# Kernel optimization log

Hardware: AMD Instinct MI355X
Metric: run time of the kernel (lower is better)

The kernel has to match this reference:

```python
import jax, jax.numpy as jnp
import numpy as np

NHEAD = 8


def _global_query_attention(cs, ks, vs):
    """cs: (B,H,G,Ek) global queries; ks: (B,H,S,Ek); vs: (B,H,S,Ev).
    For each key position i: v'_i = sum_{s<=i} softmax(K[:i] @ q) * V[:i].
    Returns (B,H,S,G,Ev)."""
    w = jnp.exp(jnp.einsum('bhge,bhse->bhgs', cs, ks))          # (B,H,G,S)
    norms = jnp.cumsum(w, axis=-1)                               # (B,H,G,S)
    wv = w[..., None] * vs[:, :, None, :, :]                     # (B,H,G,S,Ev) -- huge intermediate
    resp = jnp.cumsum(wv, axis=-2) / norms[..., None]            # (B,H,G,S,Ev)
    return jnp.swapaxes(resp, -3, -2)                            # (B,H,S,G,Ev)


def setup_inputs() -> dict:
    B, L, E, G = 4, 2048, 512, 16
    KD = VD = E
    keys = jax.random.split(jax.random.key(0), 9)
    s_qk = 0.02              # keep exp(q.k) finite in fp32
    s_v = 1.0 / np.sqrt(VD).astype(np.float32)
    return {
        'query':        jax.random.normal(keys[0], (B, L, E), jnp.float32),
        'key':          jax.random.normal(keys[1], (B, L, E), jnp.float32),
        'value':        jax.random.normal(keys[2], (B, L, E), jnp.float32),
        'context':      jax.random.normal(keys[3], (B, G, E), jnp.float32),
        'query_proj':   jax.random.normal(keys[4], (1, E, KD), jnp.float32) * s_qk,
        'key_proj':     jax.random.normal(keys[5], (1, E, KD), jnp.float32) * s_qk,
        'value_proj':   jax.random.normal(keys[6], (1, E, VD), jnp.float32) * s_v,
        'output_proj':  jax.random.normal(keys[7], (1, VD, E), jnp.float32) * s_v,
        'context_proj': jax.random.normal(keys[8], (1, E, KD), jnp.float32) * s_qk,
    }


def reference(query, key, value, context, query_proj, key_proj, value_proj, output_proj, context_proj):
    B, L, E = query.shape
    G = context.shape[1]
    H = NHEAD
    KD = query_proj.shape[-1]
    VD = value_proj.shape[-1]
    Ek, Ev = KD // H, VD // H

    def heads(x, W, n, dh):
        # (B,n,E) @ (1,E,D) -> (B,n,D) -> (B,H,n,dh)
        return jnp.swapaxes((x @ W).reshape(B, n, H, dh), 1, 2)

    cs = heads(context, context_proj, G, Ek)   # (B,H,G,Ek)
    qs = heads(query, query_proj, L, Ek)       # (B,H,L,Ek)
    ks = heads(key, key_proj, L, Ek)           # (B,H,S,Ek)
    vs = heads(value, value_proj, L, Ev)       # (B,H,S,Ev)

    resp_v = _global_query_attention(cs, ks, vs)   # (B,H,S,G,Ev)
    resp_k = _global_query_attention(cs, ks, ks)   # (B,H,S,G,Ek)

    logits = jnp.einsum('bhse,bhsge->bhsg', qs, resp_k)   # (B,H,S,G)
    w = jax.nn.softmax(logits, axis=-1)
    out = jnp.einsum('bhsg,bhsge->bhse', w, resp_v)       # (B,H,S,Ev)
    out = jnp.swapaxes(out, 1, 2).reshape(B, L, VD)       # (B,S,vdim)
    return out @ output_proj                               # (B,S,d_model)
```

## Files before the change

### kernel.cpp

```cpp
#include <hip/hip_runtime.h>
#include <hip/hip_bf16.h>

#define NB 4
#define SL 2048
#define NG 16
#define NH 8
#define DH 64
#define NBH (NB * NH)
#define NCH (SL / 64)

typedef __attribute__((ext_vector_type(8))) short bh8;
typedef __attribute__((ext_vector_type(4))) float fx4;

__device__ __forceinline__ ushort f2bf(float x) {
    union { float f; unsigned u; } v; v.f = x;
    const unsigned r = v.u + 0x7fffu + ((v.u >> 16) & 1u);
    return (ushort)(r >> 16);
}
__device__ __forceinline__ float b2f(ushort u) {
    union { unsigned u; float f; } v; v.u = ((unsigned)u) << 16;
    return v.f;
}
__device__ __forceinline__ bh8 pack8(float4 lo, float4 hi) {
    bh8 r;
    r[0] = (short)f2bf(lo.x); r[1] = (short)f2bf(lo.y);
    r[2] = (short)f2bf(lo.z); r[3] = (short)f2bf(lo.w);
    r[4] = (short)f2bf(hi.x); r[5] = (short)f2bf(hi.y);
    r[6] = (short)f2bf(hi.z); r[7] = (short)f2bf(hi.w);
    return r;
}
__device__ __forceinline__ void unpack8(bh8 v, float4& lo, float4& hi) {
    lo.x = b2f((ushort)v[0]); lo.y = b2f((ushort)v[1]);
    lo.z = b2f((ushort)v[2]); lo.w = b2f((ushort)v[3]);
    hi.x = b2f((ushort)v[4]); hi.y = b2f((ushort)v[5]);
    hi.z = b2f((ushort)v[6]); hi.w = b2f((ushort)v[7]);
}
__device__ __forceinline__ int swz(int row, int col) {
    return row * 64 + (col ^ ((row & 7) << 3));
}

__global__ __launch_bounds__(256) void convT512_4(const float* __restrict__ w0,
                                                  const float* __restrict__ w1,
                                                  const float* __restrict__ w2,
                                                  const float* __restrict__ w3,
                                                  ushort* __restrict__ o0,
                                                  ushort* __restrict__ o1,
                                                  ushort* __restrict__ o2,
                                                  ushort* __restrict__ o3) {
    const int z = blockIdx.z;
    const float* W = (z == 0) ? w0 : (z == 1) ? w1 : (z == 2) ? w2 : w3;
    ushort* WT = (z == 0) ? o0 : (z == 1) ? o1 : (z == 2) ? o2 : o3;
    __shared__ float tile[32][33];
    const int bx = blockIdx.x * 32, by = blockIdx.y * 32;
    const int tx = threadIdx.x & 31, ty = threadIdx.x >> 5;
#pragma unroll
    for (int p = 0; p < 4; ++p)
        tile[ty + p * 8][tx] = W[(size_t)(by + ty + p * 8) * 512 + bx + tx];
    __syncthreads();
#pragma unroll
    for (int p = 0; p < 4; ++p)
        WT[(size_t)(bx + ty + p * 8) * 512 + by + tx] = f2bf(tile[tx][ty + p * 8]);
}

__global__ __launch_bounds__(256, 3) void gemm_qkv_kernel(
    const float* __restrict__ qf, const float* __restrict__ kf,
    const float* __restrict__ vf, const ushort* __restrict__ qpT,
    const ushort* __restrict__ kpT, const ushort* __restrict__ vpT,
    ushort* __restrict__ qsb, ushort* __restrict__ ksb, ushort* __restrict__ vsb) {
    const int z = blockIdx.z;
    const float* A32 = (z == 0) ? qf : (z == 1) ? kf : vf;
    const ushort* BT = (z == 0) ? qpT : (z == 1) ? kpT : vpT;
    ushort* out = (z == 0) ? qsb : (z == 1) ? ksb : vsb;

    __shared__ __align__(16) ushort As[2][64 * 64];
    __shared__ __align__(16) ushort Bs[2][128 * 64];
    const int t = threadIdx.x;
    const int lane = t & 63, w = t >> 6;
    const int bm = blockIdx.x * 64, bn = blockIdx.y * 128;
    const int ar = t >> 2, ao = (t & 3) * 16;
    const size_t abase = (size_t)(bm + ar) * 512 + ao;
    const int asw0 = swz(ar, ao), asw1 = swz(ar, ao + 8);
    size_t bsrc[4];
#pragma unroll
    for (int i = 0; i < 4; ++i) {
        const int s = w * 2048 + i * 512 + lane * 8;
        const int r = s >> 6, o = (s & 63) ^ ((r & 7) << 3);
        bsrc[i] = (size_t)(bn + r) * 512 + o;
    }
    const int wr = w >> 1, wc = w & 1;
    const int fr = lane & 15, kg = lane >> 4;
    fx4 acc[2][4] = {};
    float4 a0v, a1v, a2v, a3v;

#define LOADA(kk)                                                              \
    do {                                                                       \
        a0v = *(const float4*)&A32[abase + (kk)];                              \
        a1v = *(const float4*)&A32[abase + (kk) + 4];                          \
        a2v = *(const float4*)&A32[abase + (kk) + 8];                          \
        a3v = *(const float4*)&A32[abase + (kk) + 12];                         \
    } while (0)
#define WRITEA(buf)                                                            \
    do {                                                                       \
        *(bh8*)&As[buf][asw0] = pack8(a0v, a1v);                               \
        *(bh8*)&As[buf][asw1] = pack8(a2v, a3v);                               \
    } while (0)
#define STAGEB(buf, kk)                                                        \
    do {                                                                       \
        _Pragma("unroll")                                                      \
        for (int i = 0; i < 4; ++i)                                            \
            __builtin_amdgcn_global_load_lds(                                  \
                (const __attribute__((address_space(1))) void*)(BT + bsrc[i] + (kk)), \
                (__attribute__((address_space(3))) void*)&Bs[buf][w * 2048 + i * 512], \
                16, 0, 0);                                                     \
    } while (0)

    LOADA(0);
    STAGEB(0, 0);
    WRITEA(0);
    LOADA(64);
    __syncthreads();
    int cur = 0;
    for (int k0 = 0; k0 < 512; k0 += 64) {
        if (k0 + 64 < 512) {
            STAGEB(cur ^ 1, k0 + 64);
            WRITEA(cur ^ 1);
            if (k0 + 128 < 512) LOADA(k0 + 128);
        }
#pragma unroll
        for (int kk = 0; kk < 2; ++kk) {
            bh8 af[2], bf[4];
#pragma unroll
            for (int m = 0; m < 2; ++m) {
                const int R = wr * 32 + m * 16 + fr;
                af[m] = *(const bh8*)&As[cur][swz(R, kk * 32 + kg * 8)];
            }
#pragma unroll
            for (int nn = 0; nn < 4; ++nn) {
                const int C = wc * 64 + nn * 16 + fr;
                bf[nn] = *(const bh8*)&Bs[cur][swz(C, kk * 32 + kg * 8)];
            }
#pragma unroll
            for (int m = 0; m < 2; ++m)
#pragma unroll
                for (int nn = 0; nn < 4; ++nn)
                    acc[m][nn] = __builtin_amdgcn_mfma_f32_16x16x32_bf16(
                        af[m], bf[nn], acc[m][nn], 0, 0, 0);
        }
        __syncthreads();
        cur ^= 1;
    }
#undef LOADA
#undef WRITEA
#undef STAGEB
#pragma unroll
    for (int m = 0; m < 2; ++m)
#pragma unroll
        for (int nn = 0; nn < 4; ++nn)
#pragma unroll
            for (int j = 0; j < 4; ++j) {
                const int r = bm + wr * 32 + m * 16 + kg * 4 + j;
                const int cc = bn + wc * 64 + nn * 16 + fr;
                const int b = r >> 11, i = r & 2047;
                out[(((size_t)(b * NH) + (cc >> 6)) * SL + i) * DH + (cc & 63)] =
                    f2bf(acc[m][nn][j]);
            }
}

__global__ __launch_bounds__(256, 3) void gemm_out_kernel(const ushort* __restrict__ A,
                                                          const ushort* __restrict__ BT,
                                                          float* __restrict__ out) {
    __shared__ __align__(16) ushort As[2][64 * 64];
    __shared__ __align__(16) ushort Bs[2][128 * 64];
    const int t = threadIdx.x;
    const int lane = t & 63, w = t >> 6;
    const int bm = blockIdx.x * 64, bn = blockIdx.y * 128;
    size_t asrc[2], bsrc[4];
#pragma unroll
    for (int i = 0; i < 2; ++i) {
        const int s = w * 1024 + i * 512 + lane * 8;
        const int r = s >> 6, o = (s & 63) ^ ((r & 7) << 3);
        asrc[i] = (size_t)(bm + r) * 512 + o;
    }
#pragma unroll
    for (int i = 0; i < 4; ++i) {
        const int s = w * 2048 + i * 512 + lane * 8;
        const int r = s >> 6, o = (s & 63) ^ ((r & 7) << 3);
        bsrc[i] = (size_t)(bn + r) * 512 + o;
    }
    const int wr = w >> 1, wc = w & 1;
    const int fr = lane & 15, kg = lane >> 4;
    fx4 acc[2][4] = {};

#define STAGE_O(buf, kk)                                                       \
    do {                                                                       \
        _Pragma("unroll")                                                      \
        for (int i = 0; i < 2; ++i)                                            \
            __builtin_amdgcn_global_load_lds(                                  \
                (const __attribute__((address_space(1))) void*)(A + asrc[i] + (kk)), \
                (__attribute__((address_space(3))) void*)&As[buf][w * 1024 + i * 512], \
                16, 0, 0);                                                     \
        _Pragma("unroll")                                                      \
        for (int i = 0; i < 4; ++i)                                            \
            __builtin_amdgcn_global_load_lds(                                  \
                (const __attribute__((address_space(1))) void*)(BT + bsrc[i] + (kk)), \
                (__attribute__((address_space(3))) void*)&Bs[buf][w * 2048 + i * 512], \
                16, 0, 0);                                                     \
    } while (0)

    STAGE_O(0, 0);
    __syncthreads();
    int cur = 0;
    for (int k0 = 0; k0 < 512; k0 += 64) {
        if (k0 + 64 < 512) STAGE_O(cur ^ 1, k0 + 64);
#pragma unroll
        for (int kk = 0; kk < 2; ++kk) {
            bh8 af[2], bf[4];
#pragma unroll
            for (int m = 0; m < 2; ++m) {
                const int R = wr * 32 + m * 16 + fr;
                af[m] = *(const bh8*)&As[cur][swz(R, kk * 32 + kg * 8)];
            }
#pragma unroll
            for (int nn = 0; nn < 4; ++nn) {
                const int C = wc * 64 + nn * 16 + fr;
                bf[nn] = *(const bh8*)&Bs[cur][swz(C, kk * 32 + kg * 8)];
            }
#pragma unroll
            for (int m = 0; m < 2; ++m)
#pragma unroll
                for (int nn = 0; nn < 4; ++nn)
                    acc[m][nn] = __builtin_amdgcn_mfma_f32_16x16x32_bf16(
                        af[m], bf[nn], acc[m][nn], 0, 0, 0);
        }
        __syncthreads();
        cur ^= 1;
    }
#undef STAGE_O
#pragma unroll
    for (int m = 0; m < 2; ++m)
#pragma unroll
        for (int nn = 0; nn < 4; ++nn)
#pragma unroll
            for (int j = 0; j < 4; ++j) {
                const int r = bm + wr * 32 + m * 16 + kg * 4 + j;
                const int cc = bn + wc * 64 + nn * 16 + fr;
                out[(size_t)r * 512 + cc] = acc[m][nn][j];
            }
}

template <int MODE>
__global__ __launch_bounds__(256) void gemm512(const float* __restrict__ X,
                                               const float* __restrict__ Wm,
                                               float* __restrict__ out, int n) {
    __shared__ float As[16][65];
    __shared__ float Bs[16][64];
    const int t = threadIdx.x;
    const int rm = blockIdx.x * 64;
    const int cn = blockIdx.y * 64;
    const int tm = t >> 4, tn = t & 15;
    const int arow = t >> 2, ak = (t & 3) << 2;
    const int bk = t >> 4, bc = (t & 15) << 2;
    float acc[4][4] = {};
    for (int k0 = 0; k0 < 512; k0 += 16) {
        float4 av = *(const float4*)&X[(size_t)(rm + arow) * 512 + k0 + ak];
        float4 bv = *(const float4*)&Wm[(size_t)(k0 + bk) * 512 + cn + bc];
        __syncthreads();
        As[ak + 0][arow] = av.x;
        As[ak + 1][arow] = av.y;
        As[ak + 2][arow] = av.z;
        As[ak + 3][arow] = av.w;
        *(float4*)&Bs[bk][bc] = bv;
        __syncthreads();
#pragma unroll
        for (int kk = 0; kk < 16; ++kk) {
            float a0 = As[kk][tm * 4 + 0], a1 = As[kk][tm * 4 + 1];
            float a2 = As[kk][tm * 4 + 2], a3 = As[kk][tm * 4 + 3];
            float4 b = *(const float4*)&Bs[kk][tn * 4];
            acc[0][0] += a0 * b.x; acc[0][1] += a0 * b.y; acc[0][2] += a0 * b.z; acc[0][3] += a0 * b.w;
            acc[1][0] += a1 * b.x; acc[1][1] += a1 * b.y; acc[1][2] += a1 * b.z; acc[1][3] += a1 * b.w;
            acc[2][0] += a2 * b.x; acc[2][1] += a2 * b.y; acc[2][2] += a2 * b.z; acc[2][3] += a2 * b.w;
            acc[3][0] += a3 * b.x; acc[3][1] += a3 * b.y; acc[3][2] += a3 * b.z; acc[3][3] += a3 * b.w;
        }
    }
#pragma unroll
    for (int j = 0; j < 4; ++j) {
        const int r = rm + tm * 4 + j;
#pragma unroll
        for (int jj = 0; jj < 4; ++jj) {
            const int cc = cn + tn * 4 + jj;
            if (MODE == 0) {
                const int b = r / n, i = r % n;
                out[(((size_t)(b * NH) + (cc >> 6)) * n + i) * DH + (cc & 63)] = acc[j][jj];
            } else {
                out[(size_t)r * 512 + cc] = acc[j][jj];
            }
        }
    }
}

__global__ __launch_bounds__(256) void chunk_sums_w_kernel(
    const ushort* __restrict__ ksb, const ushort* __restrict__ vsb,
    const float* __restrict__ cs, float* __restrict__ wb,
    float* __restrict__ wbT, float* __restrict__ Mc, float* __restrict__ Nc) {
    const int bh = blockIdx.x, c = blockIdx.y;
    __shared__ float Ks[64 * 64];
    __shared__ float Vs[64 * 64];
    __shared__ float Ws[64 * 16];
    __shared__ float Cs[16][65];
    const int t = threadIdx.x;
    const ushort* kbase = ksb + ((size_t)bh * SL + c * 64) * DH;
    const ushort* vbase = vsb + ((size_t)bh * SL + c * 64) * DH;
#pragma unroll
    for (int p = 0; p < 2; ++p) {
        const int idx = (p * 256 + t) * 8;
        float4 lo, hi;
        unpack8(*(const bh8*)&kbase[idx], lo, hi);
        *(float4*)&Ks[idx] = lo; *(float4*)&Ks[idx + 4] = hi;
        unpack8(*(const bh8*)&vbase[idx], lo, hi);
        *(float4*)&Vs[idx] = lo; *(float4*)&Vs[idx + 4] = hi;
    }
    {
        const int idx = t * 4;
        const float4 cv = *(const float4*)&cs[(size_t)bh * NG * DH + idx];
        const int g = idx >> 6, e = idx & 63;
        Cs[g][e + 0] = cv.x; Cs[g][e + 1] = cv.y; Cs[g][e + 2] = cv.z; Cs[g][e + 3] = cv.w;
    }
    __syncthreads();
    {
        const int i = (t * 4) >> 4, g0 = (t * 4) & 15;
        float d0 = 0.f, d1 = 0.f, d2 = 0.f, d3 = 0.f;
#pragma unroll 8
        for (int e = 0; e < 64; ++e) {
            const float kv = Ks[i * 64 + e];
            d0 += kv * Cs[g0 + 0][e];
            d1 += kv * Cs[g0 + 1][e];
            d2 += kv * Cs[g0 + 2][e];
            d3 += kv * Cs[g0 + 3][e];
        }
        float4 wv;
        wv.x = expf(d0); wv.y = expf(d1); wv.z = expf(d2); wv.w = expf(d3);
        *(float4*)&Ws[i * 16 + g0] = wv;
        *(float4*)&wb[((size_t)bh * SL + c * 64 + i) * NG + g0] = wv;
    }
    __syncthreads();
    {
        const int g = t >> 4, i0 = (t & 15) * 4;
        float4 wv4;
        wv4.x = Ws[(i0 + 0) * 16 + g];
        wv4.y = Ws[(i0 + 1) * 16 + g];
        wv4.z = Ws[(i0 + 2) * 16 + g];
        wv4.w = Ws[(i0 + 3) * 16 + g];
        *(float4*)&wbT[((size_t)(bh * NG) + g) * SL + c * 64 + i0] = wv4;
    }
    const int e = t >> 2, g0 = (t & 3) * 4;
    float m0 = 0.f, m1 = 0.f, m2 = 0.f, m3 = 0.f;
#pragma unroll 8
    for (int i = 0; i < 64; ++i) {
        const float kv = Ks[i * 64 + e];
        const float4 w = *(const float4*)&Ws[i * 16 + g0];
        m0 += kv * w.x; m1 += kv * w.y; m2 += kv * w.z; m3 += kv * w.w;
    }
    const int g2 = t >> 4, e2 = (t & 15) * 4;
    float n0 = 0.f, n1 = 0.f, n2 = 0.f, n3 = 0.f;
#pragma unroll 8
    for (int i = 0; i < 64; ++i) {
        const float wv = Ws[i * 16 + g2];
        const float4 vv = *(const float4*)&Vs[i * 64 + e2];
        n0 += wv * vv.x; n1 += wv * vv.y; n2 += wv * vv.z; n3 += wv * vv.w;
    }
    float* mo = Mc + ((size_t)(bh * NCH + c) * 64 + e) * 16 + g0;
    mo[0] = m0; mo[1] = m1; mo[2] = m2; mo[3] = m3;
    float* no = Nc + ((size_t)(bh * NCH + c) * 16 + g2) * 64 + e2;
    no[0] = n0; no[1] = n1; no[2] = n2; no[3] = n3;
}

__global__ __launch_bounds__(256) void scans_kernel(const float* __restrict__ wbT,
                                                    float* __restrict__ nb,
                                                    float* __restrict__ Mc,
                                                    float* __restrict__ Nc) {
    const int bid = blockIdx.x;
    const int t = threadIdx.x;
    if (bid < NBH * NG) {
        __shared__ float sw[2048];
        __shared__ float sp[256];
#pragma unroll
        for (int p = 0; p < 2; ++p) {
            const int idx = (p * 256 + t) * 4;
            *(float4*)&sw[idx] = *(const float4*)&wbT[(size_t)bid * SL + idx];
        }
        __syncthreads();
        float loc[8];
        float run = 0.f;
#pragma unroll
        for (int j = 0; j < 8; ++j) { run += sw[t * 8 + j]; loc[j] = run; }
        sp[t] = run;
        __syncthreads();
        for (int off = 1; off < 256; off <<= 1) {
            const float v = sp[t];
            const float add = (t >= off) ? sp[t - off] : 0.f;
            __syncthreads();
            sp[t] = v + add;
            __syncthreads();
        }
        const float offs = (t > 0) ? sp[t - 1] : 0.f;
#pragma unroll
        for (int j = 0; j < 8; ++j)
            nb[(size_t)bid * SL + t * 8 + j] = offs + loc[j];
    } else {
        const int idx = bid - NBH * NG;
        const int bh = idx >> 1;
        float* base = ((idx & 1) ? Nc : Mc) + (size_t)bh * NCH * 1024;
        float4 run = make_float4(0.f, 0.f, 0.f, 0.f);
        float4 nxt = *(float4*)&base[t * 4];
        for (int c = 0; c < NCH; ++c) {
            const float4 v = nxt;
            if (c + 1 < NCH) nxt = *(float4*)&base[(c + 1) * 1024 + t * 4];
            *(float4*)&base[c * 1024 + t * 4] = run;
            run.x += v.x; run.y += v.y; run.z += v.z; run.w += v.w;
        }
    }
}

__global__ __launch_bounds__(256) void pass1c_kernel(const ushort* __restrict__ qsb,
                                                     const ushort* __restrict__ ksb,
                                                     const float* __restrict__ wb,
                                                     const float* __restrict__ nb,
                                                     const float* __restrict__ Mc,
                                                     float* __restrict__ cb) {
    const int bh = blockIdx.x;
    const int r = blockIdx.y;
    const int s0 = r * 64;
    __shared__ float Qs[64][65];
    __shared__ float Kt[64][65];
    __shared__ float At[64][65];
    __shared__ float Wt[64 * 16];
    __shared__ float Pt[64 * 16];
    __shared__ float Lg[64][17];
    const int t = threadIdx.x;
    const int am = t >> 4, an = t & 15;
    const ushort* qbase = qsb + ((size_t)bh * SL + s0) * DH;
    const ushort* kbase = ksb + ((size_t)bh * SL + s0) * DH;
#pragma unroll
    for (int p = 0; p < 2; ++p) {
        const int idx = (p * 256 + t) * 8;
        const int row = idx >> 6, col = idx & 63;
        float4 lo, hi;
        unpack8(*(const bh8*)&qbase[idx], lo, hi);
        *(float4*)&Qs[row][col] = lo; *(float4*)&Qs[row][col + 4] = hi;
        unpack8(*(const bh8*)&kbase[idx], lo, hi);
        *(float4*)&Kt[row][col] = lo; *(float4*)&Kt[row][col + 4] = hi;
    }
    *(float4*)&Wt[t * 4] = *(const float4*)&wb[((size_t)bh * SL + s0) * NG + t * 4];
    *(float4*)&Pt[t * 4] = *(const float4*)&Mc[(size_t)(bh * NCH + r) * 1024 + t * 4];
    __syncthreads();
    float a[4][4] = {};
#pragma unroll 8
    for (int e = 0; e < 64; ++e) {
        float qv[4], kv[4];
#pragma unroll
        for (int j = 0; j < 4; ++j) qv[j] = Qs[am * 4 + j][e];
#pragma unroll
        for (int jj = 0; jj < 4; ++jj) kv[jj] = Kt[an * 4 + jj][e];
#pragma unroll
        for (int j = 0; j < 4; ++j)
#pragma unroll
            for (int jj = 0; jj < 4; ++jj) a[j][jj] += qv[j] * kv[jj];
    }
#pragma unroll
    for (int j = 0; j < 4; ++j)
#pragma unroll
        for (int jj = 0; jj < 4; ++jj) {
            if (an * 4 + jj > am * 4 + j) a[j][jj] = 0.f;
            At[am * 4 + j][an * 4 + jj] = a[j][jj];
        }
    __syncthreads();
    float lg[4] = {0.f, 0.f, 0.f, 0.f};
#pragma unroll 8
    for (int ii = 0; ii < 64; ++ii) {
        const float wv = Wt[ii * 16 + an];
#pragma unroll
        for (int j = 0; j < 4; ++j) lg[j] += At[am * 4 + j][ii] * wv;
    }
#pragma unroll 8
    for (int e = 0; e < 64; ++e) {
        const float pv = Pt[e * 16 + an];
#pragma unroll
        for (int j = 0; j < 4; ++j) lg[j] += Qs[am * 4 + j][e] * pv;
    }
#pragma unroll
    for (int j = 0; j < 4; ++j) Lg[am * 4 + j][an] = lg[j];
    __syncthreads();
    if (t < 64) {
        const int s = s0 + t;
        const float* nbase = nb + (size_t)bh * NG * SL + s;
        float nv[16], l[16];
        float mx = -1e30f;
#pragma unroll
        for (int g = 0; g < 16; ++g) {
            nv[g] = nbase[(size_t)g * SL];
            l[g] = Lg[t][g] / nv[g];
            mx = fmaxf(mx, l[g]);
        }
        float sum = 0.f;
#pragma unroll
        for (int g = 0; g < 16; ++g) { l[g] = expf(l[g] - mx); sum += l[g]; }
        const float inv = 1.f / sum;
#pragma unroll
        for (int g = 0; g < 16; ++g)
            cb[((size_t)bh * SL + s) * NG + g] = l[g] * inv / nv[g];
    }
}

__global__ __launch_bounds__(256) void pass2c_kernel(const float* __restrict__ cb,
                                                     const float* __restrict__ wb,
                                                     const ushort* __restrict__ vsb,
                                                     const float* __restrict__ Nc,
                                                     ushort* __restrict__ ohb) {
    const int bh = blockIdx.x;
    const int b = bh >> 3, h = bh & 7;
    const int r = blockIdx.y;
    const int s0 = r * 64;
    __shared__ float Ct[64][17];
    __shared__ float Wt[64][17];
    __shared__ float Vt[64 * 64];
    __shared__ float St[64][65];
    __shared__ float Ut[16 * 64];
    const int t = threadIdx.x;
    const int am = t >> 4, an = t & 15;
    {
        const int idx = t * 4;
        const int row = idx >> 4, g0 = idx & 15;
        const float4 cv = *(const float4*)&cb[((size_t)bh * SL + s0) * NG + idx];
        Ct[row][g0 + 0] = cv.x; Ct[row][g0 + 1] = cv.y;
        Ct[row][g0 + 2] = cv.z; Ct[row][g0 + 3] = cv.w;
        const float4 wv = *(const float4*)&wb[((size_t)bh * SL + s0) * NG + idx];
        Wt[row][g0 + 0] = wv.x; Wt[row][g0 + 1] = wv.y;
        Wt[row][g0 + 2] = wv.z; Wt[row][g0 + 3] = wv.w;
    }
    const ushort* vbase = vsb + ((size_t)bh * SL + s0) * DH;
#pragma unroll
    for (int p = 0; p < 2; ++p) {
        const int idx = (p * 256 + t) * 8;
        float4 lo, hi;
        unpack8(*(const bh8*)&vbase[idx], lo, hi);
        *(float4*)&Vt[idx] = lo; *(float4*)&Vt[idx + 4] = hi;
    }
    *(float4*)&Ut[t * 4] = *(const float4*)&Nc[(size_t)(bh * NCH + r) * 1024 + t * 4];
    __syncthreads();
    float sv[4][4] = {};
#pragma unroll
    for (int g = 0; g < 16; ++g) {
        float cv[4], wv[4];
#pragma unroll
        for (int j = 0; j < 4; ++j) cv[j] = Ct[am * 4 + j][g];
#pragma unroll
        for (int jj = 0; jj < 4; ++jj) wv[jj] = Wt[an * 4 + jj][g];
#pragma unroll
        for (int j = 0; j < 4; ++j)
#pragma unroll
            for (int jj = 0; jj < 4; ++jj) sv[j][jj] += cv[j] * wv[jj];
    }
#pragma unroll
    for (int j = 0; j < 4; ++j)
#pragma unroll
        for (int jj = 0; jj < 4; ++jj) {
            if (an * 4 + jj > am * 4 + j) sv[j][jj] = 0.f;
            St[am * 4 + j][an * 4 + jj] = sv[j][jj];
        }
    __syncthreads();
    float acc[4][4] = {};
#pragma unroll
    for (int g = 0; g < 16; ++g) {
        const float4 u = *(const float4*)&Ut[g * 64 + an * 4];
        float cv[4];
#pragma unroll
        for (int j = 0; j < 4; ++j) cv[j] = Ct[am * 4 + j][g];
#pragma unroll
        for (int j = 0; j < 4; ++j) {
            acc[j][0] += cv[j] * u.x; acc[j][1] += cv[j] * u.y;
            acc[j][2] += cv[j] * u.z; acc[j][3] += cv[j] * u.w;
        }
    }
#pragma unroll 8
    for (int ii = 0; ii < 64; ++ii) {
        const float4 vv = *(const float4*)&Vt[ii * 64 + an * 4];
        float st[4];
#pragma unroll
        for (int j = 0; j < 4; ++j) st[j] = St[am * 4 + j][ii];
#pragma unroll
        for (int j = 0; j < 4; ++j) {
            acc[j][0] += st[j] * vv.x; acc[j][1] += st[j] * vv.y;
            acc[j][2] += st[j] * vv.z; acc[j][3] += st[j] * vv.w;
        }
    }
#pragma unroll
    for (int j = 0; j < 4; ++j) {
        const int s = s0 + am * 4 + j;
        ushort4 pk;
        pk.x = f2bf(acc[j][0]); pk.y = f2bf(acc[j][1]);
        pk.z = f2bf(acc[j][2]); pk.w = f2bf(acc[j][3]);
        *(ushort4*)&ohb[((size_t)b * SL + s) * 512 + h * DH + an * 4] = pk;
    }
}

extern "C" void kernel_launch(void* const* d_in, const int* in_sizes, int n_in,
                              void* d_out, int out_size, void* d_ws, size_t ws_size,
                              hipStream_t stream) {
    const float* query   = (const float*)d_in[0];
    const float* key     = (const float*)d_in[1];
    const float* value   = (const float*)d_in[2];
    const float* context = (const float*)d_in[3];
    const float* qp = (const float*)d_in[4];
    const float* kp = (const float*)d_in[5];
    const float* vp = (const float*)d_in[6];
    const float* op = (const float*)d_in[7];
    const float* cp = (const float*)d_in[8];
    float* out = (float*)d_out;

    ushort* qsb = (ushort*)d_ws;
    ushort* ksb = qsb + 4194304;
    ushort* vsb = ksb + 4194304;
    ushort* ohb = vsb + 4194304;
    ushort* qpT = ohb + 4194304;
    ushort* kpT = qpT + 262144;
    ushort* vpT = kpT + 262144;
    ushort* opT = vpT + 262144;
    float* fbase = (float*)(opT + 262144);
    float* cs = fbase;
    float* wb = cs + 32768;
    float* nb = wb + 1048576;
    float* Mc = nb + 1048576;
    float* Nc = Mc + 1048576;
    float* cb = Nc + 1048576;
    float* wbT = cb + 1048576;

    dim3 blk(256);
    convT512_4<<<dim3(16, 16, 4), blk, 0, stream>>>(qp, kp, vp, op, qpT, kpT, vpT, opT);
    gemm512<0><<<dim3(1, 8), blk, 0, stream>>>(context, cp, cs, NG);
    gemm_qkv_kernel<<<dim3(128, 4, 3), blk, 0, stream>>>(query, key, value,
                                                         qpT, kpT, vpT, qsb, ksb, vsb);
    chunk_sums_w_kernel<<<dim3(NBH, NCH), blk, 0, stream>>>(ksb, vsb, cs, wb, wbT, Mc, Nc);
    scans_kernel<<<dim3(NBH * NG + NBH * 2), blk, 0, stream>>>(wbT, nb, Mc, Nc);
    pass1c_kernel<<<dim3(NBH, NCH), blk, 0, stream>>>(qsb, ksb, wb, nb, Mc, cb);
    pass2c_kernel<<<dim3(NBH, NCH), blk, 0, stream>>>(cb, wb, vsb, Nc, ohb);
    gemm_out_kernel<<<dim3(128, 4), blk, 0, stream>>>(ohb, opT, out);
}
```

Baseline: 150.3 us.

## Deepen GEMM prefetch with manual waitcnt barriers and fuse context projection into prep

Merges the context-projection GEMM into the weight transpose/convert kernel as an extra grid slice, which removes one kernel launch. In the QKV and output GEMMs it replaces __syncthreads double buffering with a two-stage prefetch. Each iteration issues the next tile's global loads after the barrier and uses explicit s_waitcnt vmcnt counts and raw s_barrier, so global latency overlaps MFMA work. The hand-tuned vmcnt counts depend on exact instruction counts, and a wrong count could race or stall.

Result: faster. 145.4 us (-3.3%).

```diff
diff --git a/kernel.cpp b/kernel.cpp
--- a/kernel.cpp
+++ b/kernel.cpp
@@ -39,27 +39,69 @@
     return row * 64 + (col ^ ((row & 7) << 3));
 }
 
-__global__ __launch_bounds__(256) void convT512_4(const float* __restrict__ w0,
-                                                  const float* __restrict__ w1,
-                                                  const float* __restrict__ w2,
-                                                  const float* __restrict__ w3,
-                                                  ushort* __restrict__ o0,
-                                                  ushort* __restrict__ o1,
-                                                  ushort* __restrict__ o2,
-                                                  ushort* __restrict__ o3) {
+__global__ __launch_bounds__(256) void prep_kernel(
+    const float* __restrict__ w0, const float* __restrict__ w1,
+    const float* __restrict__ w2, const float* __restrict__ w3,
+    const float* __restrict__ cp, const float* __restrict__ context,
+    ushort* __restrict__ o0, ushort* __restrict__ o1,
+    ushort* __restrict__ o2, ushort* __restrict__ o3,
+    float* __restrict__ cs) {
     const int z = blockIdx.z;
-    const float* W = (z == 0) ? w0 : (z == 1) ? w1 : (z == 2) ? w2 : w3;
-    ushort* WT = (z == 0) ? o0 : (z == 1) ? o1 : (z == 2) ? o2 : o3;
-    __shared__ float tile[32][33];
-    const int bx = blockIdx.x * 32, by = blockIdx.y * 32;
-    const int tx = threadIdx.x & 31, ty = threadIdx.x >> 5;
-#pragma unroll
-    for (int p = 0; p < 4; ++p)
-        tile[ty + p * 8][tx] = W[(size_t)(by + ty + p * 8) * 512 + bx + tx];
-    __syncthreads();
-#pragma unroll
-    for (int p = 0; p < 4; ++p)
-        WT[(size_t)(bx + ty + p * 8) * 512 + by + tx] = f2bf(tile[tx][ty + p * 8]);
+    const int t = threadIdx.x;
+    if (z < 4) {
+        const float* W = (z == 0) ? w0 : (z == 1) ? w1 : (z == 2) ? w2 : w3;
+        ushort* WT = (z == 0) ? o0 : (z == 1) ? o1 : (z == 2) ? o2 : o3;
+        __shared__ float tile[32][33];
+        const int bx = blockIdx.x * 32, by = blockIdx.y * 32;
+        const int tx = t & 31, ty = t >> 5;
+#pragma unroll
+        for (int p = 0; p < 4; ++p)
+            tile[ty + p * 8][tx] = W[(size_t)(by + ty + p * 8) * 512 + bx + tx];
+        __syncthreads();
+#pragma unroll
+        for (int p = 0; p < 4; ++p)
+            WT[(size_t)(bx + ty + p * 8) * 512 + by + tx] = f2bf(tile[tx][ty + p * 8]);
+    } else {
+        if (blockIdx.x != 0 || blockIdx.y >= 8) return;
+        __shared__ float As[16][65];
+        __shared__ float Bs[16][64];
+        const int cn = blockIdx.y * 64;
+        const int tm = t >> 4, tn = t & 15;
+        const int arow = t >> 2, ak = (t & 3) << 2;
+        const int bk = t >> 4, bc = (t & 15) << 2;
+        float acc[4][4] = {};
+        for (int k0 = 0; k0 < 512; k0 += 16) {
+            float4 av = *(const float4*)&context[(size_t)arow * 512 + k0 + ak];
+            float4 bv = *(const float4*)&cp[(size_t)(k0 + bk) * 512 + cn + bc];
+            __syncthreads();
+            As[ak + 0][arow] = av.x;
+            As[ak + 1][arow] = av.y;
+            As[ak + 2][arow] = av.z;
+            As[ak + 3][arow] = av.w;
+            *(float4*)&Bs[bk][bc] = bv;
+            __syncthreads();
+#pragma unroll
+            for (int kk = 0; kk < 16; ++kk) {
+                float a0 = As[kk][tm * 4 + 0], a1 = As[kk][tm * 4 + 1];
+                float a2 = As[kk][tm * 4 + 2], a3 = As[kk][tm * 4 + 3];
+                float4 b = *(const float4*)&Bs[kk][tn * 4];
+                acc[0][0] += a0 * b.x; acc[0][1] += a0 * b.y; acc[0][2] += a0 * b.z; acc[0][3] += a0 * b.w;
+                acc[1][0] += a1 * b.x; acc[1][1] += a1 * b.y; acc[1][2] += a1 * b.z; acc[1][3] += a1 * b.w;
+                acc[2][0] += a2 * b.x; acc[2][1] += a2 * b.y; acc[2][2] += a2 * b.z; acc[2][3] += a2 * b.w;
+                acc[3][0] += a3 * b.x; acc[3][1] += a3 * b.y; acc[3][2] += a3 * b.z; acc[3][3] += a3 * b.w;
+            }
+        }
+#pragma unroll
+        for (int j = 0; j < 4; ++j) {
+            const int r = tm * 4 + j;
+#pragma unroll
+            for (int jj = 0; jj < 4; ++jj) {
+                const int cc = cn + tn * 4 + jj;
+                const int b = r / NG, i = r % NG;
+                cs[(((size_t)(b * NH) + (cc >> 6)) * NG + i) * DH + (cc & 63)] = acc[j][jj];
+            }
+        }
+    }
 }
 
 __global__ __launch_bounds__(256, 3) void gemm_qkv_kernel(
@@ -113,45 +155,60 @@
                 (__attribute__((address_space(3))) void*)&Bs[buf][w * 2048 + i * 512], \
                 16, 0, 0);                                                     \
     } while (0)
+#define MFMA_PHASE(buf)                                                        \
+    do {                                                                       \
+        _Pragma("unroll")                                                      \
+        for (int kk = 0; kk < 2; ++kk) {                                       \
+            bh8 af[2], bf[4];                                                  \
+            _Pragma("unroll")                                                  \
+            for (int m = 0; m < 2; ++m) {                                      \
+                const int R = wr * 32 + m * 16 + fr;                           \
+                af[m] = *(const bh8*)&As[buf][swz(R, kk * 32 + kg * 8)];       \
+            }                                                                  \
+            _Pragma("unroll")                                                  \
+            for (int nn = 0; nn < 4; ++nn) {                                   \
+                const int C = wc * 64 + nn * 16 + fr;                          \
+                bf[nn] = *(const bh8*)&Bs[buf][swz(C, kk * 32 + kg * 8)];      \
+            }                                                                  \
+            _Pragma("unroll")                                                  \
+            for (int m = 0; m < 2; ++m)                                        \
+                _Pragma("unroll")                                              \
+                for (int nn = 0; nn < 4; ++nn)                                 \
+                    acc[m][nn] = __builtin_amdgcn_mfma_f32_16x16x32_bf16(      \
+                        af[m], bf[nn], acc[m][nn], 0, 0, 0);                   \
+        }                                                                      \
+    } while (0)
 
     LOADA(0);
     STAGEB(0, 0);
     WRITEA(0);
+    STAGEB(1, 64);
     LOADA(64);
-    __syncthreads();
+    asm volatile("s_waitcnt vmcnt(8) lgkmcnt(0)" ::: "memory");
+    __builtin_amdgcn_s_barrier();
+    __builtin_amdgcn_sched_barrier(0);
+
     int cur = 0;
     for (int k0 = 0; k0 < 512; k0 += 64) {
-        if (k0 + 64 < 512) {
-            STAGEB(cur ^ 1, k0 + 64);
-            WRITEA(cur ^ 1);
-            if (k0 + 128 < 512) LOADA(k0 + 128);
-        }
-#pragma unroll
-        for (int kk = 0; kk < 2; ++kk) {
-            bh8 af[2], bf[4];
-#pragma unroll
-            for (int m = 0; m < 2; ++m) {
-                const int R = wr * 32 + m * 16 + fr;
-                af[m] = *(const bh8*)&As[cur][swz(R, kk * 32 + kg * 8)];
-            }
-#pragma unroll
-            for (int nn = 0; nn < 4; ++nn) {
-                const int C = wc * 64 + nn * 16 + fr;
-                bf[nn] = *(const bh8*)&Bs[cur][swz(C, kk * 32 + kg * 8)];
-            }
-#pragma unroll
-            for (int m = 0; m < 2; ++m)
-#pragma unroll
-                for (int nn = 0; nn < 4; ++nn)
-                    acc[m][nn] = __builtin_amdgcn_mfma_f32_16x16x32_bf16(
-                        af[m], bf[nn], acc[m][nn], 0, 0, 0);
-        }
-        __syncthreads();
+        MFMA_PHASE(cur);
+        if (k0 + 64 < 512) WRITEA(cur ^ 1);
+        asm volatile("s_waitcnt lgkmcnt(0)" ::: "memory");
+        __builtin_amdgcn_s_barrier();
+        __builtin_amdgcn_sched_barrier(0);
+        if (k0 + 128 < 512) {
+            STAGEB(cur, k0 + 128);
+            LOADA(k0 + 128);
+            asm volatile("s_waitcnt vmcnt(8)" ::: "memory");
+        } else if (k0 + 64 < 512) {
+            asm volatile("s_waitcnt vmcnt(0)" ::: "memory");
+        }
+        __builtin_amdgcn_sched_barrier(0);
         cur ^= 1;
     }
 #undef LOADA
 #undef WRITEA
 #undef STAGEB
+#undef MFMA_PHASE
 #pragma unroll
     for (int m = 0; m < 2; ++m)
 #pragma unroll
@@ -208,10 +265,12 @@
     } while (0)
 
     STAGE_O(0, 0);
-    __syncthreads();
+    STAGE_O(1, 64);
+    asm volatile("s_waitcnt vmcnt(6)" ::: "memory");
+    __builtin_amdgcn_s_barrier();
+    __builtin_amdgcn_sched_barrier(0);
     int cur = 0;
     for (int k0 = 0; k0 < 512; k0 += 64) {
-        if (k0 + 64 < 512) STAGE_O(cur ^ 1, k0 + 64);
 #pragma unroll
         for (int kk = 0; kk < 2; ++kk) {
             bh8 af[2], bf[4];
@@ -232,7 +291,16 @@
                     acc[m][nn] = __builtin_amdgcn_mfma_f32_16x16x32_bf16(
                         af[m], bf[nn], acc[m][nn], 0, 0, 0);
         }
-        __syncthreads();
+        asm volatile("s_waitcnt lgkmcnt(0)" ::: "memory");
+        __builtin_amdgcn_s_barrier();
+        __builtin_amdgcn_sched_barrier(0);
+        if (k0 + 128 < 512) {
+            STAGE_O(cur, k0 + 128);
+            asm volatile("s_waitcnt vmcnt(6)" ::: "memory");
+        } else if (k0 + 64 < 512) {
+            asm volatile("s_waitcnt vmcnt(0)" ::: "memory");
+        }
+        __builtin_amdgcn_sched_barrier(0);
         cur ^= 1;
     }
 #undef STAGE_O
@@ -246,56 +314,6 @@
                 const int cc = bn + wc * 64 + nn * 16 + fr;
                 out[(size_t)r * 512 + cc] = acc[m][nn][j];
             }
-}
-
-template <int MODE>
-__global__ __launch_bounds__(256) void gemm512(const float* __restrict__ X,
-                                               const float* __restrict__ Wm,
-                                               float* __restrict__ out, int n) {
-    __shared__ float As[16][65];
-    __shared__ float Bs[16][64];
-    const int t = threadIdx.x;
-    const int rm = blockIdx.x * 64;
-    const int cn = blockIdx.y * 64;
-    const int tm = t >> 4, tn = t & 15;
-    const int arow = t >> 2, ak = (t & 3) << 2;
-    const int bk = t >> 4, bc = (t & 15) << 2;
-    float acc[4][4] = {};
-    for (int k0 = 0; k0 < 512; k0 += 16) {
-        float4 av = *(const float4*)&X[(size_t)(rm + arow) * 512 + k0 + ak];
-        float4 bv = *(const float4*)&Wm[(size_t)(k0 + bk) * 512 + cn + bc];
-        __syncthreads();
-        As[ak + 0][arow] = av.x;
-        As[ak + 1][arow] = av.y;
-        As[ak + 2][arow] = av.z;
-        As[ak + 3][arow] = av.w;
-        *(float4*)&Bs[bk][bc] = bv;
-        __syncthreads();
-#pragma unroll
-        for (int kk = 0; kk < 16; ++kk) {
-            float a0 = As[kk][tm * 4 + 0], a1 = As[kk][tm * 4 + 1];
-            float a2 = As[kk][tm * 4 + 2], a3 = As[kk][tm * 4 + 3];
-            float4 b = *(const float4*)&Bs[kk][tn * 4];
-            acc[0][0] += a0 * b.x; acc[0][1] += a0 * b.y; acc[0][2] += a0 * b.z; acc[0][3] += a0 * b.w;
-            acc[1][0] += a1 * b.x; acc[1][1] += a1 * b.y; acc[1][2] += a1 * b.z; acc[1][3] += a1 * b.w;
-            acc[2][0] += a2 * b.x; acc[2][1] += a2 * b.y; acc[2][2] += a2 * b.z; acc[2][3] += a2 * b.w;
-            acc[3][0] += a3 * b.x; acc[3][1] += a3 * b.y; acc[3][2] += a3 * b.z; acc[3][3] += a3 * b.w;
-        }
-    }
-#pragma unroll
-    for (int j = 0; j < 4; ++j) {
-        const int r = rm + tm * 4 + j;
-#pragma unroll
-        for (int jj = 0; jj < 4; ++jj) {
-            const int cc = cn + tn * 4 + jj;
-            if (MODE == 0) {
-                const int b = r / n, i = r % n;
-                out[(((size_t)(b * NH) + (cc >> 6)) * n + i) * DH + (cc & 63)] = acc[j][jj];
-            } else {
-                out[(size_t)r * 512 + cc] = acc[j][jj];
-            }
-        }
-    }
 }
 
 __global__ __launch_bounds__(256) void chunk_sums_w_kernel(
@@ -635,8 +653,8 @@
     float* wbT = cb + 1048576;
 
     dim3 blk(256);
-    convT512_4<<<dim3(16, 16, 4), blk, 0, stream>>>(qp, kp, vp, op, qpT, kpT, vpT, opT);
-    gemm512<0><<<dim3(1, 8), blk, 0, stream>>>(context, cp, cs, NG);
+    prep_kernel<<<dim3(16, 16, 5), blk, 0, stream>>>(qp, kp, vp, op, cp, context,
+                                                     qpT, kpT, vpT, opT, cs);
     gemm_qkv_kernel<<<dim3(128, 4, 3), blk, 0, stream>>>(query, key, value,
                                                          qpT, kpT, vpT, qsb, ksb, vsb);
     chunk_sums_w_kernel<<<dim3(NBH, NCH), blk, 0, stream>>>(ksb, vsb, cs, wb, wbT, Mc, Nc);
```
